# Performance work log

Measured on AMD Instinct MI355X. Metric: run time of the kernel, lower is better.

Reference implementation:

```python
import jax, jax.numpy as jnp
import numpy as np

EMBED_DIM = 768
NUM_HEADS = 12
HEAD_DIM = EMBED_DIM // NUM_HEADS
B, T = 2, 2048


def setup_inputs() -> dict:
    key = jax.random.key(0)
    ks = jax.random.split(key, 11)
    s = 1.0 / np.sqrt(EMBED_DIM)
    return {
        "query": jax.random.normal(ks[0], (B, T, EMBED_DIM), jnp.float32),
        "key_in": jax.random.normal(ks[1], (B, T, EMBED_DIM), jnp.float32),
        "value": jax.random.normal(ks[2], (B, T, EMBED_DIM), jnp.float32),
        "Wq": jax.random.uniform(ks[3], (EMBED_DIM, EMBED_DIM), jnp.float32, -s, s),
        "bq": jnp.zeros((EMBED_DIM,), jnp.float32),
        "Wk": jax.random.uniform(ks[4], (EMBED_DIM, EMBED_DIM), jnp.float32, -s, s),
        "bk": jnp.zeros((EMBED_DIM,), jnp.float32),
        "Wv": jax.random.uniform(ks[5], (EMBED_DIM, EMBED_DIM), jnp.float32, -s, s),
        "bv": jnp.zeros((EMBED_DIM,), jnp.float32),
        "Wo": jax.random.uniform(ks[6], (EMBED_DIM, EMBED_DIM), jnp.float32, -s, s),
        "bo": jnp.zeros((EMBED_DIM,), jnp.float32),
    }


def reference(query, key_in, value, Wq, bq, Wk, bk, Wv, bv, Wo, bo):
    b, t, _ = query.shape

    def split_heads(x):  # [B,T,E] -> [B,H,T,Dh]
        return x.reshape(b, t, NUM_HEADS, HEAD_DIM).transpose(0, 2, 1, 3)

    Q = split_heads(query @ Wq + bq)
    K = split_heads(key_in @ Wk + bk)
    V = split_heads(value @ Wv + bv)

    scores = jnp.einsum("bhqd,bhkd->bhqk", Q, K) / np.sqrt(HEAD_DIM).astype(np.float32)
    attn = jax.nn.softmax(scores, axis=-1)
    out = jnp.einsum("bhqk,bhkd->bhqd", attn, V)  # [B,H,T,Dh]
    out = out.transpose(0, 2, 1, 3).reshape(b, t, EMBED_DIM)
    return out @ Wo + bo
```

## Files before the change

kernel.cpp:

```cpp
#include <hip/hip_runtime.h>
#include <math.h>

typedef __attribute__((ext_vector_type(4))) float  floatx4;
typedef __attribute__((ext_vector_type(8))) short  short8;
typedef __attribute__((ext_vector_type(4))) short  short4v;
typedef __attribute__((ext_vector_type(8))) __bf16 bf16x8;

#define E_DIM 768
#define T_DIM 2048
#define N_B   2
#define N_H   12
#define H_D   64
#define M_TOT 4096

#define Q_SCALE 0.1803368801111204f

#if __has_builtin(__builtin_amdgcn_exp2f)
#define EXP2F(x) __builtin_amdgcn_exp2f(x)
#else
#define EXP2F(x) exp2f(x)
#endif
#if __has_builtin(__builtin_amdgcn_rcpf)
#define RCPF(x) __builtin_amdgcn_rcpf(x)
#else
#define RCPF(x) (1.0f / (x))
#endif

__device__ __forceinline__ unsigned short f32_to_bf16(float f) {
  unsigned int u = __float_as_uint(f);
  u += 0x7fffu + ((u >> 16) & 1u);
  return (unsigned short)(u >> 16);
}

__device__ __forceinline__ unsigned short f32_to_bf16_trunc(float f) {
  return (unsigned short)(__float_as_uint(f) >> 16);
}

__device__ __forceinline__ void lds_barrier() {
  asm volatile("s_waitcnt lgkmcnt(0)\n\ts_barrier" ::: "memory");
}

__device__ __forceinline__ void gload_lds16(const unsigned short* g, unsigned short* l) {
  __builtin_amdgcn_global_load_lds(
      (const __attribute__((address_space(1))) unsigned int*)(const void*)g,
      (__attribute__((address_space(3))) unsigned int*)(void*)l, 16, 0, 0);
}

__global__ __launch_bounds__(256) void convert_x(const float* __restrict__ q,
                                                 const float* __restrict__ k,
                                                 const float* __restrict__ v,
                                                 unsigned short* __restrict__ Xb) {
  const int z = blockIdx.y;
  const float* src = (z == 0) ? q : (z == 1) ? k : v;
  size_t idx = ((size_t)blockIdx.x * 256 + threadIdx.x) * 4;
  float4 val = *reinterpret_cast<const float4*>(&src[idx]);
  short4v o;
  o[0] = (short)f32_to_bf16(val.x);
  o[1] = (short)f32_to_bf16(val.y);
  o[2] = (short)f32_to_bf16(val.z);
  o[3] = (short)f32_to_bf16(val.w);
  *reinterpret_cast<short4v*>(&Xb[(size_t)z * M_TOT * E_DIM + idx]) = o;
}

__global__ __launch_bounds__(256) void transpose_w4(const float* __restrict__ W0,
                                                    const float* __restrict__ W1,
                                                    const float* __restrict__ W2,
                                                    const float* __restrict__ W3,
                                                    unsigned short* __restrict__ Wt) {
  __shared__ float tile[32][33];
  const int z = blockIdx.z;
  const float* W = (z == 0) ? W0 : (z == 1) ? W1 : (z == 2) ? W2 : W3;
  unsigned short* dst = Wt + (size_t)z * E_DIM * E_DIM;
  int k0 = blockIdx.x * 32, n0 = blockIdx.y * 32;
  int tx = threadIdx.x & 31, ty = threadIdx.x >> 5;
  for (int i = 0; i < 4; i++)
    tile[ty + i * 8][tx] = W[(size_t)(k0 + ty + i * 8) * E_DIM + n0 + tx];
  __syncthreads();
  for (int i = 0; i < 4; i++)
    dst[(size_t)(n0 + ty + i * 8) * E_DIM + k0 + tx] = f32_to_bf16(tile[tx][ty + i * 8]);
}

__global__ __launch_bounds__(256) void gemm_qkv(const unsigned short* __restrict__ Xb,
                                                const unsigned short* __restrict__ WtAll,
                                                const float* __restrict__ bq,
                                                const float* __restrict__ bk,
                                                const float* __restrict__ bv,
                                                unsigned short* __restrict__ outQKV) {
  __shared__ unsigned short As[128 * 32];
  __shared__ unsigned short Bs[128 * 32];

  const int z = blockIdx.z;
  const unsigned short* A = Xb + (size_t)z * M_TOT * E_DIM;
  const float* bias = (z == 0) ? bq : (z == 1) ? bk : bv;
  const unsigned short* W = WtAll + (size_t)z * E_DIM * E_DIM;
  unsigned short* out = outQKV + (size_t)z * M_TOT * E_DIM;
  const float scale = (z == 0) ? Q_SCALE : 1.0f;

  const int tid = threadIdx.x;
  const int lane = tid & 63, wv = tid >> 6;
  const int m15 = lane & 15, quad = lane >> 4;
  const int wm = (wv & 1) * 64, wn = (wv >> 1) * 64;
  const int m0 = blockIdx.x * 128, n0 = blockIdx.y * 128;

  floatx4 acc[4][4] = {};
  const int srow = lane >> 2, scol = (lane & 3) * 8;

  for (int k0 = 0; k0 < E_DIM; k0 += 32) {
    for (int cc = 0; cc < 2; cc++) {
      int c = wv * 2 + cc;
      gload_lds16(&A[(size_t)(m0 + c * 16 + srow) * E_DIM + k0 + scol], &As[c * 512]);
      gload_lds16(&W[(size_t)(n0 + c * 16 + srow) * E_DIM + k0 + scol], &Bs[c * 512]);
    }
    __syncthreads();
    bf16x8 af[4], bfr[4];
    for (int i = 0; i < 4; i++)
      af[i] = *reinterpret_cast<const bf16x8*>(&As[(wm + i * 16 + m15) * 32 + quad * 8]);
    for (int j = 0; j < 4; j++)
      bfr[j] = *reinterpret_cast<const bf16x8*>(&Bs[(wn + j * 16 + m15) * 32 + quad * 8]);
    for (int i = 0; i < 4; i++)
      for (int j = 0; j < 4; j++)
        acc[i][j] = __builtin_amdgcn_mfma_f32_16x16x32_bf16(af[i], bfr[j], acc[i][j], 0, 0, 0);
    __syncthreads();
  }

  for (int i = 0; i < 4; i++)
    for (int j = 0; j < 4; j++) {
      int gn = n0 + wn + j * 16 + m15;
      int h = gn >> 6, d = gn & 63;
      float bso = bias[gn];
      for (int r = 0; r < 4; r++) {
        int gm = m0 + wm + i * 16 + quad * 4 + r;
        int bb = gm >> 11, tt = gm & 2047;
        float v = (acc[i][j][r] + bso) * scale;
        out[(((size_t)bb * N_H + h) * T_DIM + tt) * H_D + d] = f32_to_bf16(v);
      }
    }
}

__global__ __launch_bounds__(256) void transpose_v(const unsigned short* __restrict__ Vg_all,
                                                   unsigned short* __restrict__ VT) {
  __shared__ unsigned short tile[64 * 72];
  const int t0 = blockIdx.x * 64, h = blockIdx.y, bb = blockIdx.z;
  const unsigned short* Vg = Vg_all + (((size_t)bb * N_H + h) * T_DIM) * H_D;
  unsigned short* VTh = VT + (((size_t)bb * N_H + h) * H_D) * T_DIM;
  const int tid = threadIdx.x;
  const int tloc = tid & 63, d0 = (tid >> 6) * 16;

  short8 r0 = *reinterpret_cast<const short8*>(&Vg[(size_t)(t0 + tloc) * H_D + d0]);
  short8 r1 = *reinterpret_cast<const short8*>(&Vg[(size_t)(t0 + tloc) * H_D + d0 + 8]);
#pragma unroll
  for (int j = 0; j < 8; j++) {
    tile[(d0 + j) * 72 + tloc] = (unsigned short)r0[j];
    tile[(d0 + 8 + j) * 72 + tloc] = (unsigned short)r1[j];
  }
  __syncthreads();
  const int d = tid >> 2, ts = (tid & 3) * 16;
  short8 w0 = *reinterpret_cast<const short8*>(&tile[d * 72 + ts]);
  short8 w1 = *reinterpret_cast<const short8*>(&tile[d * 72 + ts + 8]);
  *reinterpret_cast<short8*>(&VTh[(size_t)d * T_DIM + t0 + ts]) = w0;
  *reinterpret_cast<short8*>(&VTh[(size_t)d * T_DIM + t0 + ts + 8]) = w1;
}

__global__ __launch_bounds__(256) void attn(const unsigned short* __restrict__ QKV,
                                            const unsigned short* __restrict__ VT,
                                            unsigned short* __restrict__ ctx) {
  __shared__ unsigned short Qs[64 * 72];
  __shared__ unsigned short Sb[64 * 72];
  __shared__ unsigned short Ks[64 * 72];
  __shared__ unsigned short Vs[2][64 * 72];

  const int qt = blockIdx.x, h = blockIdx.y, bb = blockIdx.z;
  const size_t headoff = (((size_t)bb * N_H + h) * T_DIM) * H_D;
  const unsigned short* Qg = QKV + headoff;
  const unsigned short* Kg = QKV + (size_t)M_TOT * E_DIM + headoff;
  const unsigned short* VTg = VT + (((size_t)bb * N_H + h) * H_D) * T_DIM;

  const int tid = threadIdx.x, lane = tid & 63, wv = tid >> 6;
  const int m15 = lane & 15, quad = lane >> 4;
  const int q0 = qt * 64;
  const int rs = tid >> 3, cs = (tid & 7) * 8;

  for (int p = 0; p < 2; p++)
    *reinterpret_cast<short8*>(&Qs[(p * 32 + rs) * 72 + cs]) =
        *reinterpret_cast<const short8*>(&Qg[(size_t)(q0 + p * 32 + rs) * H_D + cs]);

  short8 kreg[2], vreg[2];
  for (int p = 0; p < 2; p++) {
    kreg[p] = *reinterpret_cast<const short8*>(&Kg[(size_t)(p * 32 + rs) * H_D + cs]);
    vreg[p] = *reinterpret_cast<const short8*>(&VTg[(size_t)(p * 32 + rs) * T_DIM + cs]);
  }
  lds_barrier();

  bf16x8 aq[2];
  aq[0] = *reinterpret_cast<const bf16x8*>(&Qs[(wv * 16 + m15) * 72 + 0 + quad * 8]);
  aq[1] = *reinterpret_cast<const bf16x8*>(&Qs[(wv * 16 + m15) * 72 + 32 + quad * 8]);

  for (int p = 0; p < 2; p++) {
    *reinterpret_cast<short8*>(&Ks[(p * 32 + rs) * 72 + cs]) = kreg[p];
    *reinterpret_cast<short8*>(&Vs[0][(p * 32 + rs) * 72 + cs]) = vreg[p];
  }
  for (int p = 0; p < 2; p++) {
    kreg[p] = *reinterpret_cast<const short8*>(&Kg[(size_t)(64 + p * 32 + rs) * H_D + cs]);
    vreg[p] = *reinterpret_cast<const short8*>(&VTg[(size_t)(p * 32 + rs) * T_DIM + 64 + cs]);
  }
  lds_barrier();

  floatx4 o[4] = {};
  floatx4 lacc = {};
  const short8 ones_s = {0x3f80, 0x3f80, 0x3f80, 0x3f80, 0x3f80, 0x3f80, 0x3f80, 0x3f80};
  const bf16x8 onesb = __builtin_bit_cast(bf16x8, ones_s);
  unsigned short* stripA = &Qs[wv * 16 * 72];
  unsigned short* stripB = &Sb[wv * 16 * 72];

  {
    floatx4 s[4] = {};
    for (int kk = 0; kk < 2; kk++)
      for (int j = 0; j < 4; j++) {
        bf16x8 b = *reinterpret_cast<const bf16x8*>(&Ks[(j * 16 + m15) * 72 + kk * 32 + quad * 8]);
        s[j] = __builtin_amdgcn_mfma_f32_16x16x32_bf16(aq[kk], b, s[j], 0, 0, 0);
      }
    lds_barrier();
    for (int p = 0; p < 2; p++) {
      *reinterpret_cast<short8*>(&Ks[(p * 32 + rs) * 72 + cs]) = kreg[p];
      *reinterpret_cast<short8*>(&Vs[1][(p * 32 + rs) * 72 + cs]) = vreg[p];
    }
    for (int p = 0; p < 2; p++) {
      kreg[p] = *reinterpret_cast<const short8*>(&Kg[(size_t)(128 + p * 32 + rs) * H_D + cs]);
      vreg[p] = *reinterpret_cast<const short8*>(&VTg[(size_t)(p * 32 + rs) * T_DIM + 128 + cs]);
    }
    for (int j = 0; j < 4; j++)
      for (int r = 0; r < 4; r++)
        stripA[(quad * 4 + r) * 72 + j * 16 + m15] = f32_to_bf16_trunc(EXP2F(s[j][r]));
  }

  for (int kt = 1; kt < 32; kt++) {
    unsigned short* sp_prev = (kt & 1) ? stripA : stripB;
    unsigned short* sp_cur = (kt & 1) ? stripB : stripA;
    const unsigned short* vprev = Vs[(kt - 1) & 1];
    lds_barrier();

    for (int kk = 0; kk < 2; kk++) {
      bf16x8 a = *reinterpret_cast<const bf16x8*>(&sp_prev[m15 * 72 + kk * 32 + quad * 8]);
      lacc = __builtin_amdgcn_mfma_f32_16x16x32_bf16(a, onesb, lacc, 0, 0, 0);
      for (int j = 0; j < 4; j++) {
        bf16x8 b = *reinterpret_cast<const bf16x8*>(&vprev[(j * 16 + m15) * 72 + kk * 32 + quad * 8]);
        o[j] = __builtin_amdgcn_mfma_f32_16x16x32_bf16(a, b, o[j], 0, 0, 0);
      }
    }

    floatx4 s[4] = {};
    for (int kk = 0; kk < 2; kk++)
      for (int j = 0; j < 4; j++) {
        bf16x8 b = *reinterpret_cast<const bf16x8*>(&Ks[(j * 16 + m15) * 72 + kk * 32 + quad * 8]);
        s[j] = __builtin_amdgcn_mfma_f32_16x16x32_bf16(aq[kk], b, s[j], 0, 0, 0);
      }
    lds_barrier();

    if (kt < 31) {
      for (int p = 0; p < 2; p++) {
        *reinterpret_cast<short8*>(&Ks[(p * 32 + rs) * 72 + cs]) = kreg[p];
        *reinterpret_cast<short8*>(&Vs[(kt + 1) & 1][(p * 32 + rs) * 72 + cs]) = vreg[p];
      }
      if (kt < 30)
        for (int p = 0; p < 2; p++) {
          kreg[p] = *reinterpret_cast<const short8*>(&Kg[(size_t)((kt + 2) * 64 + p * 32 + rs) * H_D + cs]);
          vreg[p] = *reinterpret_cast<const short8*>(&VTg[(size_t)(p * 32 + rs) * T_DIM + (kt + 2) * 64 + cs]);
        }
    }

    for (int j = 0; j < 4; j++)
      for (int r = 0; r < 4; r++)
        sp_cur[(quad * 4 + r) * 72 + j * 16 + m15] = f32_to_bf16_trunc(EXP2F(s[j][r]));
  }

  asm volatile("s_waitcnt lgkmcnt(0)" ::: "memory");
  for (int kk = 0; kk < 2; kk++) {
    bf16x8 a = *reinterpret_cast<const bf16x8*>(&stripB[m15 * 72 + kk * 32 + quad * 8]);
    lacc = __builtin_amdgcn_mfma_f32_16x16x32_bf16(a, onesb, lacc, 0, 0, 0);
    for (int j = 0; j < 4; j++) {
      bf16x8 b = *reinterpret_cast<const bf16x8*>(&Vs[1][(j * 16 + m15) * 72 + kk * 32 + quad * 8]);
      o[j] = __builtin_amdgcn_mfma_f32_16x16x32_bf16(a, b, o[j], 0, 0, 0);
    }
  }

  for (int r = 0; r < 4; r++) {
    float rl = RCPF(lacc[r]);
    int q = q0 + wv * 16 + quad * 4 + r;
    for (int j = 0; j < 4; j++)
      ctx[(size_t)(bb * T_DIM + q) * E_DIM + h * 64 + j * 16 + m15] = f32_to_bf16(o[j][r] * rl);
  }
}

__global__ __launch_bounds__(256) void gemm_out(const unsigned short* __restrict__ Actx,
                                                const unsigned short* __restrict__ Wt,
                                                const float* __restrict__ bias,
                                                float* __restrict__ out) {
  __shared__ unsigned short As[64 * 32];
  __shared__ unsigned short Bs[128 * 32];

  const int tid = threadIdx.x;
  const int lane = tid & 63, wv = tid >> 6;
  const int m15 = lane & 15, quad = lane >> 4;
  const int wm = (wv & 1) * 32, wn = (wv >> 1) * 64;
  const int m0 = blockIdx.x * 64, n0 = blockIdx.y * 128;

  floatx4 acc[2][4] = {};
  const int srow = lane >> 2, scol = (lane & 3) * 8;

  for (int k0 = 0; k0 < E_DIM; k0 += 32) {
    gload_lds16(&Actx[(size_t)(m0 + wv * 16 + srow) * E_DIM + k0 + scol], &As[wv * 512]);
    for (int cc = 0; cc < 2; cc++) {
      int c = wv * 2 + cc;
      gload_lds16(&Wt[(size_t)(n0 + c * 16 + srow) * E_DIM + k0 + scol], &Bs[c * 512]);
    }
    __syncthreads();
    bf16x8 af[2], bfr[4];
    for (int i = 0; i < 2; i++)
      af[i] = *reinterpret_cast<const bf16x8*>(&As[(wm + i * 16 + m15) * 32 + quad * 8]);
    for (int j = 0; j < 4; j++)
      bfr[j] = *reinterpret_cast<const bf16x8*>(&Bs[(wn + j * 16 + m15) * 32 + quad * 8]);
    for (int i = 0; i < 2; i++)
      for (int j = 0; j < 4; j++)
        acc[i][j] = __builtin_amdgcn_mfma_f32_16x16x32_bf16(af[i], bfr[j], acc[i][j], 0, 0, 0);
    __syncthreads();
  }

  for (int i = 0; i < 2; i++)
    for (int j = 0; j < 4; j++) {
      int gn = n0 + wn + j * 16 + m15;
      float bso = bias[gn];
      for (int r = 0; r < 4; r++) {
        int gm = m0 + wm + i * 16 + quad * 4 + r;
        out[(size_t)gm * E_DIM + gn] = acc[i][j][r] + bso;
      }
    }
}

extern "C" void kernel_launch(void* const* d_in, const int* in_sizes, int n_in,
                              void* d_out, int out_size, void* d_ws, size_t ws_size,
                              hipStream_t stream) {
  const float* query  = (const float*)d_in[0];
  const float* key_in = (const float*)d_in[1];
  const float* value  = (const float*)d_in[2];
  const float* Wq = (const float*)d_in[3];
  const float* bq = (const float*)d_in[4];
  const float* Wk = (const float*)d_in[5];
  const float* bk = (const float*)d_in[6];
  const float* Wv = (const float*)d_in[7];
  const float* bv = (const float*)d_in[8];
  const float* Wo = (const float*)d_in[9];
  const float* bo = (const float*)d_in[10];
  float* out = (float*)d_out;

  unsigned short* ws  = (unsigned short*)d_ws;
  unsigned short* Wt  = ws;
  unsigned short* Xb  = Wt + (size_t)4 * E_DIM * E_DIM;
  unsigned short* QKV = Xb + (size_t)3 * M_TOT * E_DIM;
  unsigned short* VT  = QKV + (size_t)3 * M_TOT * E_DIM;
  unsigned short* ctx = VT + (size_t)N_B * N_H * H_D * T_DIM;

  dim3 tb(256);
  convert_x<<<dim3(M_TOT * E_DIM / 1024, 3), tb, 0, stream>>>(query, key_in, value, Xb);
  transpose_w4<<<dim3(24, 24, 4), tb, 0, stream>>>(Wq, Wk, Wv, Wo, Wt);

  gemm_qkv<<<dim3(32, 6, 3), tb, 0, stream>>>(Xb, Wt, bq, bk, bv, QKV);
  transpose_v<<<dim3(32, 12, 2), tb, 0, stream>>>(QKV + (size_t)2 * M_TOT * E_DIM, VT);
  attn<<<dim3(32, 12, 2), tb, 0, stream>>>(QKV, VT, ctx);
  gemm_out<<<dim3(64, 6), tb, 0, stream>>>(ctx, Wt + (size_t)3 * E_DIM * E_DIM, bo, out);
  (void)in_sizes; (void)n_in; (void)out_size; (void)ws_size;
}
```

Before: 200.6 us.

## Rewrite attention kernel with 32x32 MFMA, register-resident P, and async LDS loads

Rewrites the attention kernel to use 2 waves of 128 threads, each handling 32 query rows with 32x32x16 bf16 MFMAs. It computes S transposed, so exp'd probabilities are packed with v_cvt_pk_bf16 and permlane32 swaps into A-operands directly in registers instead of round-tripping through LDS strips. K/V tiles are double-buffered via global_load_lds with an XOR-swizzled layout. The row sum is accumulated in scalar registers instead of an MFMA against ones. This cuts LDS traffic and instruction count per tile, at the cost of fewer threads per block and more registers per thread.

Measured after the change: 205.3 us. 2.4% more time.

```diff
diff --git a/kernel.cpp b/kernel.cpp
--- a/kernel.cpp
+++ b/kernel.cpp
@@ -2,9 +2,11 @@
 #include <math.h>
 
 typedef __attribute__((ext_vector_type(4))) float  floatx4;
+typedef __attribute__((ext_vector_type(16))) float f32x16;
 typedef __attribute__((ext_vector_type(8))) short  short8;
 typedef __attribute__((ext_vector_type(4))) short  short4v;
 typedef __attribute__((ext_vector_type(8))) __bf16 bf16x8;
+typedef __attribute__((ext_vector_type(4))) unsigned int uint4v;
 
 #define E_DIM 768
 #define T_DIM 2048
@@ -32,10 +34,6 @@
   return (unsigned short)(u >> 16);
 }
 
-__device__ __forceinline__ unsigned short f32_to_bf16_trunc(float f) {
-  return (unsigned short)(__float_as_uint(f) >> 16);
-}
-
 __device__ __forceinline__ void lds_barrier() {
   asm volatile("s_waitcnt lgkmcnt(0)\n\ts_barrier" ::: "memory");
 }
@@ -44,6 +42,16 @@
   __builtin_amdgcn_global_load_lds(
       (const __attribute__((address_space(1))) unsigned int*)(const void*)g,
       (__attribute__((address_space(3))) unsigned int*)(void*)l, 16, 0, 0);
+}
+
+__device__ __forceinline__ unsigned int cvtpk_bf16(float lo, float hi) {
+  unsigned int r;
+  asm("v_cvt_pk_bf16_f32 %0, %1, %2" : "=v"(r) : "v"(lo), "v"(hi));
+  return r;
+}
+
+__device__ __forceinline__ void perml32_swap(unsigned int& a, unsigned int& b) {
+  asm volatile("v_permlane32_swap_b32 %0, %1" : "+v"(a), "+v"(b));
 }
 
 __global__ __launch_bounds__(256) void convert_x(const float* __restrict__ q,
@@ -161,13 +169,11 @@
   *reinterpret_cast<short8*>(&VTh[(size_t)d * T_DIM + t0 + ts + 8]) = w1;
 }
 
-__global__ __launch_bounds__(256) void attn(const unsigned short* __restrict__ QKV,
+__global__ __launch_bounds__(128) void attn(const unsigned short* __restrict__ QKV,
                                             const unsigned short* __restrict__ VT,
                                             unsigned short* __restrict__ ctx) {
-  __shared__ unsigned short Qs[64 * 72];
-  __shared__ unsigned short Sb[64 * 72];
-  __shared__ unsigned short Ks[64 * 72];
-  __shared__ unsigned short Vs[2][64 * 72];
+  __shared__ unsigned short Ks[2][64 * 64];
+  __shared__ unsigned short Vs[2][64 * 64];
 
   const int qt = blockIdx.x, h = blockIdx.y, bb = blockIdx.z;
   const size_t headoff = (((size_t)bb * N_H + h) * T_DIM) * H_D;
@@ -175,119 +181,122 @@
   const unsigned short* Kg = QKV + (size_t)M_TOT * E_DIM + headoff;
   const unsigned short* VTg = VT + (((size_t)bb * N_H + h) * H_D) * T_DIM;
 
-  const int tid = threadIdx.x, lane = tid & 63, wv = tid >> 6;
-  const int m15 = lane & 15, quad = lane >> 4;
-  const int q0 = qt * 64;
-  const int rs = tid >> 3, cs = (tid & 7) * 8;
-
-  for (int p = 0; p < 2; p++)
-    *reinterpret_cast<short8*>(&Qs[(p * 32 + rs) * 72 + cs]) =
-        *reinterpret_cast<const short8*>(&Qg[(size_t)(q0 + p * 32 + rs) * H_D + cs]);
-
-  short8 kreg[2], vreg[2];
-  for (int p = 0; p < 2; p++) {
-    kreg[p] = *reinterpret_cast<const short8*>(&Kg[(size_t)(p * 32 + rs) * H_D + cs]);
-    vreg[p] = *reinterpret_cast<const short8*>(&VTg[(size_t)(p * 32 + rs) * T_DIM + cs]);
-  }
+  const int tid = threadIdx.x;
+  const int lane = tid & 63, wv = tid >> 6;
+  const int l31 = lane & 31, hi = lane >> 5, l7 = lane & 7;
+  const int q0 = qt * 64 + wv * 32;
+
+  const int srow = lane >> 3;
+  const int sslot = (lane & 7) ^ srow;
+  const unsigned short* gK = Kg + (size_t)srow * H_D + sslot * 8;
+  const unsigned short* gV = VTg + (size_t)srow * T_DIM + sslot * 8;
+
+  bf16x8 aq[4];
+#pragma unroll
+  for (int c = 0; c < 4; c++)
+    aq[c] = *reinterpret_cast<const bf16x8*>(&Qg[(size_t)(q0 + l31) * H_D + c * 16 + hi * 8]);
+
+#pragma unroll
+  for (int i = 0; i < 8; i++) {
+    if (wv == 0) gload_lds16(gK + (size_t)(i * 8) * H_D, &Ks[0][i * 512]);
+    else         gload_lds16(gV + (size_t)(i * 8) * T_DIM, &Vs[0][i * 512]);
+  }
+#pragma unroll
+  for (int i = 0; i < 8; i++) {
+    if (wv == 0) gload_lds16(gK + (size_t)(64 + i * 8) * H_D, &Ks[1][i * 512]);
+    else         gload_lds16(gV + (size_t)(i * 8) * T_DIM + 64, &Vs[1][i * 512]);
+  }
+  asm volatile("s_waitcnt vmcnt(0)" ::: "memory");
   lds_barrier();
 
-  bf16x8 aq[2];
-  aq[0] = *reinterpret_cast<const bf16x8*>(&Qs[(wv * 16 + m15) * 72 + 0 + quad * 8]);
-  aq[1] = *reinterpret_cast<const bf16x8*>(&Qs[(wv * 16 + m15) * 72 + 32 + quad * 8]);
-
-  for (int p = 0; p < 2; p++) {
-    *reinterpret_cast<short8*>(&Ks[(p * 32 + rs) * 72 + cs]) = kreg[p];
-    *reinterpret_cast<short8*>(&Vs[0][(p * 32 + rs) * 72 + cs]) = vreg[p];
-  }
-  for (int p = 0; p < 2; p++) {
-    kreg[p] = *reinterpret_cast<const short8*>(&Kg[(size_t)(64 + p * 32 + rs) * H_D + cs]);
-    vreg[p] = *reinterpret_cast<const short8*>(&VTg[(size_t)(p * 32 + rs) * T_DIM + 64 + cs]);
-  }
-  lds_barrier();
-
-  floatx4 o[4] = {};
-  floatx4 lacc = {};
-  const short8 ones_s = {0x3f80, 0x3f80, 0x3f80, 0x3f80, 0x3f80, 0x3f80, 0x3f80, 0x3f80};
-  const bf16x8 onesb = __builtin_bit_cast(bf16x8, ones_s);
-  unsigned short* stripA = &Qs[wv * 16 * 72];
-  unsigned short* stripB = &Sb[wv * 16 * 72];
-
-  {
-    floatx4 s[4] = {};
-    for (int kk = 0; kk < 2; kk++)
-      for (int j = 0; j < 4; j++) {
-        bf16x8 b = *reinterpret_cast<const bf16x8*>(&Ks[(j * 16 + m15) * 72 + kk * 32 + quad * 8]);
-        s[j] = __builtin_amdgcn_mfma_f32_16x16x32_bf16(aq[kk], b, s[j], 0, 0, 0);
-      }
+  f32x16 o0 = {}, o1 = {};
+  float lacc = 0.f;
+
+  for (int kt = 0; kt < 32; ++kt) {
+    const unsigned short* kb = Ks[kt & 1];
+    const unsigned short* vb = Vs[kt & 1];
+
+    f32x16 s0 = {}, s1 = {};
+#pragma unroll
+    for (int c = 0; c < 4; c++) {
+      const int slot = ((c << 1) | hi) ^ l7;
+      bf16x8 k0 = *reinterpret_cast<const bf16x8*>(&kb[l31 * 64 + slot * 8]);
+      bf16x8 k1 = *reinterpret_cast<const bf16x8*>(&kb[(32 + l31) * 64 + slot * 8]);
+      s0 = __builtin_amdgcn_mfma_f32_32x32x16_bf16(k0, aq[c], s0, 0, 0, 0);
+      s1 = __builtin_amdgcn_mfma_f32_32x32x16_bf16(k1, aq[c], s1, 0, 0, 0);
+    }
+
+#pragma unroll
+    for (int i = 0; i < 16; i++) { s0[i] = EXP2F(s0[i]); s1[i] = EXP2F(s1[i]); }
+    float ps = 0.f;
+#pragma unroll
+    for (int i = 0; i < 16; i++) ps += s0[i] + s1[i];
+    lacc += ps;
+
+    bf16x8 pa0[2], pa1[2];
+#pragma unroll
+    for (int cc = 0; cc < 2; cc++) {
+      {
+        unsigned int x0 = cvtpk_bf16(s0[8 * cc + 0], s0[8 * cc + 1]);
+        unsigned int x1 = cvtpk_bf16(s0[8 * cc + 2], s0[8 * cc + 3]);
+        unsigned int y0 = cvtpk_bf16(s0[8 * cc + 4], s0[8 * cc + 5]);
+        unsigned int y1 = cvtpk_bf16(s0[8 * cc + 6], s0[8 * cc + 7]);
+        perml32_swap(x0, y0);
+        perml32_swap(x1, y1);
+        uint4v u; u[0] = x0; u[1] = x1; u[2] = y0; u[3] = y1;
+        pa0[cc] = __builtin_bit_cast(bf16x8, u);
+      }
+      {
+        unsigned int x0 = cvtpk_bf16(s1[8 * cc + 0], s1[8 * cc + 1]);
+        unsigned int x1 = cvtpk_bf16(s1[8 * cc + 2], s1[8 * cc + 3]);
+        unsigned int y0 = cvtpk_bf16(s1[8 * cc + 4], s1[8 * cc + 5]);
+        unsigned int y1 = cvtpk_bf16(s1[8 * cc + 6], s1[8 * cc + 7]);
+        perml32_swap(x0, y0);
+        perml32_swap(x1, y1);
+        uint4v u; u[0] = x0; u[1] = x1; u[2] = y0; u[3] = y1;
+        pa1[cc] = __builtin_bit_cast(bf16x8, u);
+      }
+    }
+
+#pragma unroll
+    for (int cc = 0; cc < 2; cc++) {
+      const int sl0 = ((cc << 1) | hi) ^ l7;
+      const int sl1 = (4 + (cc << 1) + hi) ^ l7;
+      bf16x8 v00 = *reinterpret_cast<const bf16x8*>(&vb[l31 * 64 + sl0 * 8]);
+      bf16x8 v01 = *reinterpret_cast<const bf16x8*>(&vb[(32 + l31) * 64 + sl0 * 8]);
+      bf16x8 v10 = *reinterpret_cast<const bf16x8*>(&vb[l31 * 64 + sl1 * 8]);
+      bf16x8 v11 = *reinterpret_cast<const bf16x8*>(&vb[(32 + l31) * 64 + sl1 * 8]);
+      o0 = __builtin_amdgcn_mfma_f32_32x32x16_bf16(pa0[cc], v00, o0, 0, 0, 0);
+      o1 = __builtin_amdgcn_mfma_f32_32x32x16_bf16(pa0[cc], v01, o1, 0, 0, 0);
+      o0 = __builtin_amdgcn_mfma_f32_32x32x16_bf16(pa1[cc], v10, o0, 0, 0, 0);
+      o1 = __builtin_amdgcn_mfma_f32_32x32x16_bf16(pa1[cc], v11, o1, 0, 0, 0);
+    }
+
+    if (kt == 31) break;
     lds_barrier();
-    for (int p = 0; p < 2; p++) {
-      *reinterpret_cast<short8*>(&Ks[(p * 32 + rs) * 72 + cs]) = kreg[p];
-      *reinterpret_cast<short8*>(&Vs[1][(p * 32 + rs) * 72 + cs]) = vreg[p];
-    }
-    for (int p = 0; p < 2; p++) {
-      kreg[p] = *reinterpret_cast<const short8*>(&Kg[(size_t)(128 + p * 32 + rs) * H_D + cs]);
-      vreg[p] = *reinterpret_cast<const short8*>(&VTg[(size_t)(p * 32 + rs) * T_DIM + 128 + cs]);
-    }
-    for (int j = 0; j < 4; j++)
-      for (int r = 0; r < 4; r++)
-        stripA[(quad * 4 + r) * 72 + j * 16 + m15] = f32_to_bf16_trunc(EXP2F(s[j][r]));
-  }
-
-  for (int kt = 1; kt < 32; kt++) {
-    unsigned short* sp_prev = (kt & 1) ? stripA : stripB;
-    unsigned short* sp_cur = (kt & 1) ? stripB : stripA;
-    const unsigned short* vprev = Vs[(kt - 1) & 1];
+    if (kt < 30) {
+      const int nt = kt + 2;
+#pragma unroll
+      for (int i = 0; i < 8; i++) {
+        if (wv == 0) gload_lds16(gK + (size_t)(nt * 64 + i * 8) * H_D, &Ks[kt & 1][i * 512]);
+        else         gload_lds16(gV + (size_t)(i * 8) * T_DIM + nt * 64, &Vs[kt & 1][i * 512]);
+      }
+      asm volatile("s_waitcnt vmcnt(8)" ::: "memory");
+    } else {
+      asm volatile("s_waitcnt vmcnt(0)" ::: "memory");
+    }
     lds_barrier();
-
-    for (int kk = 0; kk < 2; kk++) {
-      bf16x8 a = *reinterpret_cast<const bf16x8*>(&sp_prev[m15 * 72 + kk * 32 + quad * 8]);
-      lacc = __builtin_amdgcn_mfma_f32_16x16x32_bf16(a, onesb, lacc, 0, 0, 0);
-      for (int j = 0; j < 4; j++) {
-        bf16x8 b = *reinterpret_cast<const bf16x8*>(&vprev[(j * 16 + m15) * 72 + kk * 32 + quad * 8]);
-        o[j] = __builtin_amdgcn_mfma_f32_16x16x32_bf16(a, b, o[j], 0, 0, 0);
-      }
-    }
-
-    floatx4 s[4] = {};
-    for (int kk = 0; kk < 2; kk++)
-      for (int j = 0; j < 4; j++) {
-        bf16x8 b = *reinterpret_cast<const bf16x8*>(&Ks[(j * 16 + m15) * 72 + kk * 32 + quad * 8]);
-        s[j] = __builtin_amdgcn_mfma_f32_16x16x32_bf16(aq[kk], b, s[j], 0, 0, 0);
-      }
-    lds_barrier();
-
-    if (kt < 31) {
-      for (int p = 0; p < 2; p++) {
-        *reinterpret_cast<short8*>(&Ks[(p * 32 + rs) * 72 + cs]) = kreg[p];
-        *reinterpret_cast<short8*>(&Vs[(kt + 1) & 1][(p * 32 + rs) * 72 + cs]) = vreg[p];
-      }
-      if (kt < 30)
-        for (int p = 0; p < 2; p++) {
-          kreg[p] = *reinterpret_cast<const short8*>(&Kg[(size_t)((kt + 2) * 64 + p * 32 + rs) * H_D + cs]);
-          vreg[p] = *reinterpret_cast<const short8*>(&VTg[(size_t)(p * 32 + rs) * T_DIM + (kt + 2) * 64 + cs]);
-        }
-    }
-
-    for (int j = 0; j < 4; j++)
-      for (int r = 0; r < 4; r++)
-        sp_cur[(quad * 4 + r) * 72 + j * 16 + m15] = f32_to_bf16_trunc(EXP2F(s[j][r]));
-  }
-
-  asm volatile("s_waitcnt lgkmcnt(0)" ::: "memory");
-  for (int kk = 0; kk < 2; kk++) {
-    bf16x8 a = *reinterpret_cast<const bf16x8*>(&stripB[m15 * 72 + kk * 32 + quad * 8]);
-    lacc = __builtin_amdgcn_mfma_f32_16x16x32_bf16(a, onesb, lacc, 0, 0, 0);
-    for (int j = 0; j < 4; j++) {
-      bf16x8 b = *reinterpret_cast<const bf16x8*>(&Vs[1][(j * 16 + m15) * 72 + kk * 32 + quad * 8]);
-      o[j] = __builtin_amdgcn_mfma_f32_16x16x32_bf16(a, b, o[j], 0, 0, 0);
-    }
-  }
-
-  for (int r = 0; r < 4; r++) {
-    float rl = RCPF(lacc[r]);
-    int q = q0 + wv * 16 + quad * 4 + r;
-    for (int j = 0; j < 4; j++)
-      ctx[(size_t)(bb * T_DIM + q) * E_DIM + h * 64 + j * 16 + m15] = f32_to_bf16(o[j][r] * rl);
+  }
+
+  float ltot = lacc + __shfl_xor(lacc, 32, 64);
+  float rl = RCPF(ltot);
+  const size_t obase = ((size_t)bb * T_DIM + q0) * E_DIM + (size_t)h * H_D;
+#pragma unroll
+  for (int r = 0; r < 16; r++) {
+    const int qrow = (r & 3) + 8 * (r >> 2) + 4 * hi;
+    float rq = __shfl(rl, qrow, 64);
+    ctx[obase + (size_t)qrow * E_DIM + l31]      = f32_to_bf16(o0[r] * rq);
+    ctx[obase + (size_t)qrow * E_DIM + 32 + l31] = f32_to_bf16(o1[r] * rq);
   }
 }
 
@@ -365,7 +374,7 @@
 
   gemm_qkv<<<dim3(32, 6, 3), tb, 0, stream>>>(Xb, Wt, bq, bk, bv, QKV);
   transpose_v<<<dim3(32, 12, 2), tb, 0, stream>>>(QKV + (size_t)2 * M_TOT * E_DIM, VT);
-  attn<<<dim3(32, 12, 2), tb, 0, stream>>>(QKV, VT, ctx);
+  attn<<<dim3(32, 12, 2), dim3(128), 0, stream>>>(QKV, VT, ctx);
   gemm_out<<<dim3(64, 6), tb, 0, stream>>>(ctx, Wt + (size_t)3 * E_DIM * E_DIM, bo, out);
   (void)in_sizes; (void)n_in; (void)out_size; (void)ws_size;
 }
```
